# Optimization experiments

Hardware: AMD Instinct MI355X
Metric: run time of the kernel (lower is better)

The kernel has to match this reference:

```python
import jax, jax.numpy as jnp
import numpy as np
import math

S, B, D = 2048, 8, 256
HEADS = 8
DPROJ = 128
DFF = 1024
DH = DPROJ // HEADS  # 16


def _layernorm(x, g, b, eps=1e-5):
    mu = jnp.mean(x, axis=-1, keepdims=True)
    var = jnp.mean((x - mu) ** 2, axis=-1, keepdims=True)
    return (x - mu) * jax.lax.rsqrt(var + eps) * g + b


def setup_inputs() -> dict:
    key = jax.random.key(0)
    ks = jax.random.split(key, 16)
    s = 0.02
    return {
        "src": jax.random.normal(ks[0], (S, B, D), dtype=jnp.float32),
        "Wq": jax.random.normal(ks[1], (D, DPROJ), dtype=jnp.float32) * s,
        "bq": jnp.zeros((DPROJ,), dtype=jnp.float32),
        "Wk": jax.random.normal(ks[2], (D, DPROJ), dtype=jnp.float32) * s,
        "bk": jnp.zeros((DPROJ,), dtype=jnp.float32),
        "Wv": jax.random.normal(ks[3], (D, DPROJ), dtype=jnp.float32) * s,
        "bv": jnp.zeros((DPROJ,), dtype=jnp.float32),
        "Wo": jax.random.normal(ks[4], (DPROJ, D), dtype=jnp.float32) * s,
        "ln1_g": jnp.ones((D,), dtype=jnp.float32),
        "ln1_b": jnp.zeros((D,), dtype=jnp.float32),
        "W1": jax.random.normal(ks[5], (D, DFF), dtype=jnp.float32) * s,
        "b1": jnp.zeros((DFF,), dtype=jnp.float32),
        "W2": jax.random.normal(ks[6], (DFF, D), dtype=jnp.float32) * s,
        "b2": jnp.zeros((D,), dtype=jnp.float32),
        "ln2_g": jnp.ones((D,), dtype=jnp.float32),
        "ln2_b": jnp.zeros((D,), dtype=jnp.float32),
    }


def reference(src, Wq, bq, Wk, bk, Wv, bv, Wo, ln1_g, ln1_b, W1, b1, W2, b2, ln2_g, ln2_b):
    # src: (S, B, D)
    q = src @ Wq + bq  # (S, B, DPROJ)
    k = src @ Wk + bk
    v = src @ Wv + bv

    # _reshape_to_batches: (S, B, h*dh) -> (S, B*h, dh), then sdpa moves batch first
    def split_heads(x):
        return jnp.transpose(x.reshape(S, B * HEADS, DH), (1, 0, 2))  # (B*h, S, dh)

    qh, kh, vh = split_heads(q), split_heads(k), split_heads(v)
    scores = jnp.einsum('bid,bjd->bij', qh, kh) / math.sqrt(DH)  # (B*h, S, S)
    attn = jax.nn.softmax(scores, axis=-1)
    ctx = jnp.einsum('bij,bjd->bid', attn, vh)  # (B*h, S, dh)

    # _reshape_from_batches: (B*h, S, dh) -> (S, B, DPROJ)
    ctx = jnp.transpose(ctx, (1, 0, 2)).reshape(S, B, DPROJ)
    y = ctx @ Wo  # (S, B, D), no bias

    x = _layernorm(src + y, ln1_g, ln1_b)
    ffn = jax.nn.relu(x @ W1 + b1) @ W2 + b2
    return _layernorm(x + ffn, ln2_g, ln2_b)
```

## Files before the change

### kernel.cpp

```cpp
#include <hip/hip_runtime.h>
#include <math.h>

#define SLEN 2048
#define BATCH 8
#define DMODEL 256
#define HEADS 8
#define DPROJ 128
#define DFF 1024
#define DH 16
#define MROWS (SLEN*BATCH)

typedef unsigned short u16;
typedef unsigned int u32;
typedef __attribute__((ext_vector_type(8))) short short8;
typedef __attribute__((ext_vector_type(4))) short short4v;
typedef __attribute__((ext_vector_type(4))) float f32x4;
typedef __attribute__((ext_vector_type(4))) unsigned short u16x4;

__device__ __forceinline__ u16 f2bf(float x) {
    union { float f; u32 u; } v; v.f = x;
    u32 r = v.u + 0x7FFFu + ((v.u >> 16) & 1u);
    return (u16)(r >> 16);
}
__device__ __forceinline__ float bf2f(u16 h) {
    union { u32 u; float f; } v; v.u = ((u32)h) << 16;
    return v.f;
}
__device__ __forceinline__ float fexp2(float x) { return __builtin_amdgcn_exp2f(x); }
__device__ __forceinline__ short8 lds_short8_b64(const u16* p) {
    short4v lo = *(const short4v*)p;
    short4v hi = *(const short4v*)(p + 4);
    return __builtin_shufflevector(lo, hi, 0, 1, 2, 3, 4, 5, 6, 7);
}

__global__ void conv_src_kernel(const float* __restrict__ src, u16* __restrict__ dst) {
    int idx = (blockIdx.x * 256 + threadIdx.x) * 4;
    float4 v = *(const float4*)(src + idx);
    u16x4 o;
    o.x = f2bf(v.x); o.y = f2bf(v.y); o.z = f2bf(v.z); o.w = f2bf(v.w);
    *(u16x4*)(dst + idx) = o;
}

__global__ void conv_wts_kernel(const float* __restrict__ Wq, const float* __restrict__ Wk,
                                const float* __restrict__ Wv, const float* __restrict__ Wo,
                                const float* __restrict__ W1, const float* __restrict__ W2,
                                u16* __restrict__ WqT, u16* __restrict__ WkT,
                                u16* __restrict__ WvT, u16* __restrict__ WoT,
                                u16* __restrict__ W1T, u16* __restrict__ W2T) {
    int i = blockIdx.x * 256 + threadIdx.x;
    if (i < 32768) {
        int n = i >> 8, k = i & 255;
        WqT[i] = f2bf(Wq[k * 128 + n]);
    } else if (i < 65536) {
        int j = i - 32768; int n = j >> 8, k = j & 255;
        WkT[j] = f2bf(Wk[k * 128 + n]);
    } else if (i < 98304) {
        int j = i - 65536; int n = j >> 8, k = j & 255;
        WvT[j] = f2bf(Wv[k * 128 + n]);
    } else if (i < 131072) {
        int j = i - 98304; int n = j >> 7, k = j & 127;
        WoT[j] = f2bf(Wo[k * 256 + n]);
    } else if (i < 393216) {
        int j = i - 131072; int n = j >> 8, k = j & 255;
        W1T[j] = f2bf(W1[k * 1024 + n]);
    } else if (i < 655360) {
        int j = i - 393216; int n = j >> 10, k = j & 1023;
        W2T[j] = f2bf(W2[k * 256 + n]);
    }
}

template<int BN, bool RELU, bool HAS_BIAS, bool OUT_BF16>
__global__ void mfma_gemm(const u16* __restrict__ A, const u16* __restrict__ BT,
                          const float* __restrict__ bias, void* __restrict__ Cout,
                          int M, int N, int K) {
    constexpr int NJ = BN / 32;
    __shared__ __align__(16) u16 As[128 * 40];
    __shared__ __align__(16) u16 Bs[BN * 40];
    const int tid = threadIdx.x;
    const int row0 = blockIdx.x * 128;
    const int col0 = blockIdx.y * BN;
    const int w = tid >> 6, l = tid & 63;
    const int wr = (w & 1) * 64, wc = (w >> 1) * (BN / 2);
    const int lcol = l & 15, lrow = (l >> 4) * 4, kq = (l >> 4) * 8;
    const int sr = tid >> 2;
    const int sc = (tid & 3) * 8;

    f32x4 acc[4][NJ] = {};
    for (int k0 = 0; k0 < K; k0 += 32) {
        *(uint4*)(As + sr * 40 + sc) =
            *(const uint4*)(A + (size_t)(row0 + sr) * K + k0 + sc);
        *(uint4*)(As + (sr + 64) * 40 + sc) =
            *(const uint4*)(A + (size_t)(row0 + sr + 64) * K + k0 + sc);
        *(uint4*)(Bs + sr * 40 + sc) =
            *(const uint4*)(BT + (size_t)(col0 + sr) * K + k0 + sc);
        if (BN == 128)
            *(uint4*)(Bs + (sr + 64) * 40 + sc) =
                *(const uint4*)(BT + (size_t)(col0 + sr + 64) * K + k0 + sc);
        __syncthreads();
        short8 af[4], bf[NJ];
        #pragma unroll
        for (int i = 0; i < 4; ++i)
            af[i] = *(const short8*)(As + (wr + i * 16 + lcol) * 40 + kq);
        #pragma unroll
        for (int j = 0; j < NJ; ++j)
            bf[j] = *(const short8*)(Bs + (wc + j * 16 + lcol) * 40 + kq);
        #pragma unroll
        for (int i = 0; i < 4; ++i)
            #pragma unroll
            for (int j = 0; j < NJ; ++j)
                acc[i][j] = __builtin_amdgcn_mfma_f32_16x16x32_bf16(
                    af[i], bf[j], acc[i][j], 0, 0, 0);
        __syncthreads();
    }
    float bv[NJ];
    #pragma unroll
    for (int j = 0; j < NJ; ++j)
        bv[j] = HAS_BIAS ? bias[col0 + wc + j * 16 + lcol] : 0.f;
    #pragma unroll
    for (int i = 0; i < 4; ++i) {
        #pragma unroll
        for (int r = 0; r < 4; ++r) {
            size_t grow = row0 + wr + i * 16 + lrow + r;
            #pragma unroll
            for (int j = 0; j < NJ; ++j) {
                int gcol = col0 + wc + j * 16 + lcol;
                float c = acc[i][j][r] + bv[j];
                if (RELU) c = fmaxf(c, 0.f);
                if (OUT_BF16) ((u16*)Cout)[grow * N + gcol] = f2bf(c);
                else          ((float*)Cout)[grow * N + gcol] = c;
            }
        }
    }
}

__global__ void qkv_mfma(const u16* __restrict__ A,
                         const u16* __restrict__ WqT, const u16* __restrict__ WkT,
                         const u16* __restrict__ WvT,
                         const float* __restrict__ bq, const float* __restrict__ bk,
                         const float* __restrict__ bv,
                         u16* __restrict__ qhp, u16* __restrict__ khp,
                         u16* __restrict__ vhb) {
    const int which = blockIdx.z;
    const u16* BT   = which == 0 ? WqT : (which == 1 ? WkT : WvT);
    const float* bs = which == 0 ? bq : (which == 1 ? bk : bv);
    const float scale = which == 0 ? 0.25f * 1.44269504f : 1.0f;
    __shared__ __align__(16) u16 As[128 * 40];
    __shared__ __align__(16) u16 Bs[128 * 40];
    const int tid = threadIdx.x;
    const int row0 = blockIdx.x * 128;
    const int w = tid >> 6, l = tid & 63;
    const int wr = (w & 1) * 64, wc = (w >> 1) * 64;
    const int lcol = l & 15, lrow = (l >> 4) * 4, kq = (l >> 4) * 8;
    const int sr = tid >> 2;
    const int sc = (tid & 3) * 8;

    f32x4 acc[4][4] = {};
    for (int k0 = 0; k0 < DMODEL; k0 += 32) {
        *(uint4*)(As + sr * 40 + sc) =
            *(const uint4*)(A + (size_t)(row0 + sr) * DMODEL + k0 + sc);
        *(uint4*)(As + (sr + 64) * 40 + sc) =
            *(const uint4*)(A + (size_t)(row0 + sr + 64) * DMODEL + k0 + sc);
        *(uint4*)(Bs + sr * 40 + sc) =
            *(const uint4*)(BT + (size_t)sr * DMODEL + k0 + sc);
        *(uint4*)(Bs + (sr + 64) * 40 + sc) =
            *(const uint4*)(BT + (size_t)(sr + 64) * DMODEL + k0 + sc);
        __syncthreads();
        short8 af[4], bf[4];
        #pragma unroll
        for (int i = 0; i < 4; ++i)
            af[i] = *(const short8*)(As + (wr + i * 16 + lcol) * 40 + kq);
        #pragma unroll
        for (int j = 0; j < 4; ++j)
            bf[j] = *(const short8*)(Bs + (wc + j * 16 + lcol) * 40 + kq);
        #pragma unroll
        for (int i = 0; i < 4; ++i)
            #pragma unroll
            for (int j = 0; j < 4; ++j)
                acc[i][j] = __builtin_amdgcn_mfma_f32_16x16x32_bf16(
                    af[i], bf[j], acc[i][j], 0, 0, 0);
        __syncthreads();
    }
    #pragma unroll
    for (int i = 0; i < 4; ++i) {
        #pragma unroll
        for (int r = 0; r < 4; ++r) {
            int grow = row0 + wr + i * 16 + lrow + r;
            int b = grow & 7, s = grow >> 3;
            #pragma unroll
            for (int j = 0; j < 4; ++j) {
                int gcol = wc + j * 16 + lcol;
                int h = gcol >> 4, d = gcol & 15;
                float c = acc[i][j][r] + bs[gcol];
                if (which == 2) {
                    vhb[((size_t)(b * 8 + h) * SLEN + s) * 16 + d] = f2bf(c);
                } else {
                    u16* base = (which == 0 ? qhp : khp)
                              + ((size_t)(b * 8 + h) * SLEN + s) * 32;
                    base[d] = f2bf(c * scale);
                    base[d + 16] = 0;
                }
            }
        }
    }
}

__global__ __launch_bounds__(256, 4)
void attn_mfma(const u16* __restrict__ qg, const u16* __restrict__ kg,
               const u16* __restrict__ vg, u16* __restrict__ ctx) {
    __shared__ __align__(16) u16 Qs[128 * 40];
    __shared__ __align__(16) u16 Ksm[64 * 40];
    __shared__ __align__(16) u16 VTs[16 * 68];
    __shared__ __align__(16) u16 Ps[4 * 32 * 68];
    const int bh = blockIdx.y;
    const int q0 = blockIdx.x * 128;
    const int tid = threadIdx.x;
    const int w = tid >> 6, l = tid & 63;
    const int lcol = l & 15, lrow4 = (l >> 4) * 4, kq = (l >> 4) * 8;
    u16* Pw = Ps + w * (32 * 68);

    {
        const u16* qbase = qg + ((size_t)bh * SLEN + q0) * 32;
        #pragma unroll
        for (int it = 0; it < 2; ++it) {
            int idx = tid + it * 256;
            int row = idx >> 2, c = (idx & 3) * 8;
            *(uint4*)(Qs + row * 40 + c) = *(const uint4*)(qbase + row * 32 + c);
        }
    }

    f32x4 o_[2] = {};
    f32x4 ls[2] = {};
    const short one_bf = (short)0x3F80;
    short8 onesB = {one_bf, one_bf, one_bf, one_bf, one_bf, one_bf, one_bf, one_bf};

    const int srow = tid >> 2, sc8 = (tid & 3) * 8;
    const int vkey = tid & 63, vd4 = (tid >> 6) * 4;

    for (int k0 = 0; k0 < SLEN; k0 += 64) {
        __syncthreads();
        *(uint4*)(Ksm + srow * 40 + sc8) =
            *(const uint4*)(kg + ((size_t)bh * SLEN + k0 + srow) * 32 + sc8);
        {
            uint2 vv = *(const uint2*)(vg + ((size_t)bh * SLEN + k0 + vkey) * 16 + vd4);
            VTs[(vd4 + 0) * 68 + vkey] = (u16)(vv.x & 0xffff);
            VTs[(vd4 + 1) * 68 + vkey] = (u16)(vv.x >> 16);
            VTs[(vd4 + 2) * 68 + vkey] = (u16)(vv.y & 0xffff);
            VTs[(vd4 + 3) * 68 + vkey] = (u16)(vv.y >> 16);
        }
        __syncthreads();

        short8 aq[2];
        #pragma unroll
        for (int mi = 0; mi < 2; ++mi)
            aq[mi] = *(const short8*)(Qs + (w * 32 + mi * 16 + lcol) * 40 + kq);
        f32x4 s_[2][4];
        #pragma unroll
        for (int nj = 0; nj < 4; ++nj) {
            short8 bk_ = *(const short8*)(Ksm + (nj * 16 + lcol) * 40 + kq);
            #pragma unroll
            for (int mi = 0; mi < 2; ++mi) {
                f32x4 z = {0.f, 0.f, 0.f, 0.f};
                s_[mi][nj] = __builtin_amdgcn_mfma_f32_16x16x32_bf16(aq[mi], bk_, z, 0, 0, 0);
            }
        }
        #pragma unroll
        for (int mi = 0; mi < 2; ++mi)
            #pragma unroll
            for (int nj = 0; nj < 4; ++nj)
                #pragma unroll
                for (int r = 0; r < 4; ++r)
                    Pw[(mi * 16 + lrow4 + r) * 68 + nj * 16 + lcol] =
                        f2bf(fexp2(s_[mi][nj][r]));
        #pragma unroll
        for (int ks = 0; ks < 2; ++ks) {
            short8 bv_ = lds_short8_b64(VTs + lcol * 68 + ks * 32 + kq);
            #pragma unroll
            for (int mi = 0; mi < 2; ++mi) {
                short8 ap = lds_short8_b64(Pw + (mi * 16 + lcol) * 68 + ks * 32 + kq);
                o_[mi] = __builtin_amdgcn_mfma_f32_16x16x32_bf16(ap, bv_, o_[mi], 0, 0, 0);
                ls[mi] = __builtin_amdgcn_mfma_f32_16x16x32_bf16(ap, onesB, ls[mi], 0, 0, 0);
            }
        }
    }
    const int b = bh >> 3, h = bh & 7;
    #pragma unroll
    for (int mi = 0; mi < 2; ++mi)
        #pragma unroll
        for (int r = 0; r < 4; ++r) {
            int qrow = q0 + w * 32 + mi * 16 + lrow4 + r;
            ctx[((size_t)qrow * BATCH + b) * DPROJ + h * DH + lcol] =
                f2bf(o_[mi][r] / ls[mi][r]);
        }
}

__global__ void ln1_kernel(const float* __restrict__ src, const u16* __restrict__ y,
                           const float* __restrict__ g, const float* __restrict__ bb,
                           u16* __restrict__ xb) {
    const int w = threadIdx.x >> 6, l = threadIdx.x & 63;
    const int row = blockIdx.x * 4 + w;
    const int c = l * 4;
    size_t base = (size_t)row * DMODEL;
    float4 s4 = *(const float4*)(src + base + c);
    u16x4 y4 = *(const u16x4*)(y + base + c);
    float v[4] = { s4.x + bf2f(y4.x), s4.y + bf2f(y4.y),
                   s4.z + bf2f(y4.z), s4.w + bf2f(y4.w) };
    float sum = v[0] + v[1] + v[2] + v[3];
    float ss  = v[0]*v[0] + v[1]*v[1] + v[2]*v[2] + v[3]*v[3];
    #pragma unroll
    for (int off = 1; off < 64; off <<= 1) {
        sum += __shfl_xor(sum, off);
        ss  += __shfl_xor(ss, off);
    }
    float mu = sum * (1.0f / 256.0f);
    float var = ss * (1.0f / 256.0f) - mu * mu;
    float rs = rsqrtf(var + 1e-5f);
    float4 g4 = *(const float4*)(g + c);
    float4 b4 = *(const float4*)(bb + c);
    u16x4 o;
    o.x = f2bf((v[0] - mu) * rs * g4.x + b4.x);
    o.y = f2bf((v[1] - mu) * rs * g4.y + b4.y);
    o.z = f2bf((v[2] - mu) * rs * g4.z + b4.z);
    o.w = f2bf((v[3] - mu) * rs * g4.w + b4.w);
    *(u16x4*)(xb + base + c) = o;
}

__global__ void ln2_kernel(const u16* __restrict__ x, const u16* __restrict__ f,
                           const float* __restrict__ g, const float* __restrict__ bb,
                           float* __restrict__ out) {
    const int w = threadIdx.x >> 6, l = threadIdx.x & 63;
    const int row = blockIdx.x * 4 + w;
    const int c = l * 4;
    size_t base = (size_t)row * DMODEL;
    u16x4 x4 = *(const u16x4*)(x + base + c);
    u16x4 f4 = *(const u16x4*)(f + base + c);
    float v[4] = { bf2f(x4.x) + bf2f(f4.x), bf2f(x4.y) + bf2f(f4.y),
                   bf2f(x4.z) + bf2f(f4.z), bf2f(x4.w) + bf2f(f4.w) };
    float sum = v[0] + v[1] + v[2] + v[3];
    float ss  = v[0]*v[0] + v[1]*v[1] + v[2]*v[2] + v[3]*v[3];
    #pragma unroll
    for (int off = 1; off < 64; off <<= 1) {
        sum += __shfl_xor(sum, off);
        ss  += __shfl_xor(ss, off);
    }
    float mu = sum * (1.0f / 256.0f);
    float var = ss * (1.0f / 256.0f) - mu * mu;
    float rs = rsqrtf(var + 1e-5f);
    float4 g4 = *(const float4*)(g + c);
    float4 b4 = *(const float4*)(bb + c);
    float4 o;
    o.x = (v[0] - mu) * rs * g4.x + b4.x;
    o.y = (v[1] - mu) * rs * g4.y + b4.y;
    o.z = (v[2] - mu) * rs * g4.z + b4.z;
    o.w = (v[3] - mu) * rs * g4.w + b4.w;
    *(float4*)(out + base + c) = o;
}

extern "C" void kernel_launch(void* const* d_in, const int* in_sizes, int n_in,
                              void* d_out, int out_size, void* d_ws, size_t ws_size,
                              hipStream_t stream) {
    const float* src = (const float*)d_in[0];
    const float* Wq  = (const float*)d_in[1];
    const float* bq  = (const float*)d_in[2];
    const float* Wk  = (const float*)d_in[3];
    const float* bk  = (const float*)d_in[4];
    const float* Wv  = (const float*)d_in[5];
    const float* bv  = (const float*)d_in[6];
    const float* Wo  = (const float*)d_in[7];
    const float* g1  = (const float*)d_in[8];
    const float* be1 = (const float*)d_in[9];
    const float* W1  = (const float*)d_in[10];
    const float* b1  = (const float*)d_in[11];
    const float* W2  = (const float*)d_in[12];
    const float* b2  = (const float*)d_in[13];
    const float* g2  = (const float*)d_in[14];
    const float* be2 = (const float*)d_in[15];
    char* ws = (char*)d_ws;
    float* out = (float*)d_out;

    u16* qhp  = (u16*)(ws + 0);
    u16* khp  = (u16*)(ws + 8388608);
    u16* vhb  = (u16*)(ws + 16777216);
    u16* ctxb = (u16*)(ws + 20971520);
    u16* yb   = (u16*)(ws + 25165824);
    u16* hb   = (u16*)(ws + 0);
    u16* xb   = (u16*)(ws + 33554432);
    u16* fb   = (u16*)(ws + 41943040);
    u16* srcb = (u16*)(ws + 50331648);
    u16* WqT  = (u16*)(ws + 58720256);
    u16* WkT  = (u16*)(ws + 58785792);
    u16* WvT  = (u16*)(ws + 58851328);
    u16* WoT  = (u16*)(ws + 58916864);
    u16* W1T  = (u16*)(ws + 58982400);
    u16* W2T  = (u16*)(ws + 59506688);

    conv_src_kernel<<<4096, 256, 0, stream>>>(src, srcb);
    conv_wts_kernel<<<2560, 256, 0, stream>>>(Wq, Wk, Wv, Wo, W1, W2,
                                              WqT, WkT, WvT, WoT, W1T, W2T);
    qkv_mfma<<<dim3(128, 1, 3), 256, 0, stream>>>(srcb, WqT, WkT, WvT,
                                                  bq, bk, bv, qhp, khp, vhb);
    attn_mfma<<<dim3(16, 64), 256, 0, stream>>>(qhp, khp, vhb, ctxb);
    mfma_gemm<64, false, false, true><<<dim3(128, 4), 256, 0, stream>>>(
        ctxb, WoT, nullptr, yb, MROWS, DMODEL, DPROJ);
    ln1_kernel<<<MROWS / 4, 256, 0, stream>>>(src, yb, g1, be1, xb);
    mfma_gemm<128, true, true, true><<<dim3(128, 8), 256, 0, stream>>>(
        xb, W1T, b1, hb, MROWS, DFF, DMODEL);
    mfma_gemm<64, false, true, true><<<dim3(128, 4), 256, 0, stream>>>(
        hb, W2T, b2, fb, MROWS, DMODEL, DFF);
    ln2_kernel<<<MROWS / 4, 256, 0, stream>>>(xb, fb, g2, be2, out);
}
```

Measured before the change: 246.9 us.

## Load attention K/V fragments directly from global and pre-transpose V

Adds a separate kernel that transposes V into a per-head [d][key] layout. The attention kernel now loads Q, K and V MFMA fragments straight from global memory into registers, dropping the shared-memory K/V staging and both block-wide barriers per key tile. It computes S^T (K as the A operand) so the exp'd probabilities can be packed two bf16 per u32 with a perm instruction and written to LDS as wider stores. The cost is an extra kernel launch plus the V transpose traffic, and uncoalesced, repeated global (L2) fragment loads by every wave.

```diff
diff --git a/kernel.cpp b/kernel.cpp
--- a/kernel.cpp
+++ b/kernel.cpp
@@ -13,7 +13,6 @@
 typedef unsigned short u16;
 typedef unsigned int u32;
 typedef __attribute__((ext_vector_type(8))) short short8;
-typedef __attribute__((ext_vector_type(4))) short short4v;
 typedef __attribute__((ext_vector_type(4))) float f32x4;
 typedef __attribute__((ext_vector_type(4))) unsigned short u16x4;
 
@@ -22,15 +21,10 @@
     u32 r = v.u + 0x7FFFu + ((v.u >> 16) & 1u);
     return (u16)(r >> 16);
 }
-__device__ __forceinline__ float bf2f(u16 h) {
-    union { u32 u; float f; } v; v.u = ((u32)h) << 16;
-    return v.f;
-}
 __device__ __forceinline__ float fexp2(float x) { return __builtin_amdgcn_exp2f(x); }
-__device__ __forceinline__ short8 lds_short8_b64(const u16* p) {
-    short4v lo = *(const short4v*)p;
-    short4v hi = *(const short4v*)(p + 4);
-    return __builtin_shufflevector(lo, hi, 0, 1, 2, 3, 4, 5, 6, 7);
+__device__ __forceinline__ u32 pack_bf(float lo, float hi) {
+    union { float f; u32 u; } a, b; a.f = lo; b.f = hi;
+    return __builtin_amdgcn_perm(b.u, a.u, 0x07060302u);
 }
 
 __global__ void conv_src_kernel(const float* __restrict__ src, u16* __restrict__ dst) {
@@ -204,95 +198,109 @@
     }
 }
 
+__global__ void transpose_v(const u16* __restrict__ vhb, u16* __restrict__ vT) {
+    __shared__ u16 T[128 * 24];
+    const int bh = blockIdx.y;
+    const int c0 = blockIdx.x * 128;
+    const int t = threadIdx.x;
+    {
+        int key = t >> 1, half = t & 1;
+        *(uint4*)(T + key * 24 + half * 8) =
+            *(const uint4*)(vhb + ((size_t)bh * SLEN + c0 + key) * 16 + half * 8);
+    }
+    __syncthreads();
+    int d = t >> 4, k8 = (t & 15) * 8;
+    u16x4 o0, o1;
+    o0.x = T[(k8 + 0) * 24 + d]; o0.y = T[(k8 + 1) * 24 + d];
+    o0.z = T[(k8 + 2) * 24 + d]; o0.w = T[(k8 + 3) * 24 + d];
+    o1.x = T[(k8 + 4) * 24 + d]; o1.y = T[(k8 + 5) * 24 + d];
+    o1.z = T[(k8 + 6) * 24 + d]; o1.w = T[(k8 + 7) * 24 + d];
+    u16* dst = vT + ((size_t)bh * 16 + d) * SLEN + c0 + k8;
+    *(u16x4*)dst = o0;
+    *(u16x4*)(dst + 4) = o1;
+}
+
 __global__ __launch_bounds__(256, 4)
 void attn_mfma(const u16* __restrict__ qg, const u16* __restrict__ kg,
-               const u16* __restrict__ vg, u16* __restrict__ ctx) {
-    __shared__ __align__(16) u16 Qs[128 * 40];
-    __shared__ __align__(16) u16 Ksm[64 * 40];
-    __shared__ __align__(16) u16 VTs[16 * 68];
-    __shared__ __align__(16) u16 Ps[4 * 32 * 68];
+               const u16* __restrict__ vT, u16* __restrict__ ctx) {
+    __shared__ __align__(16) u16 Ps[4 * 32 * 70];
     const int bh = blockIdx.y;
     const int q0 = blockIdx.x * 128;
     const int tid = threadIdx.x;
     const int w = tid >> 6, l = tid & 63;
-    const int lcol = l & 15, lrow4 = (l >> 4) * 4, kq = (l >> 4) * 8;
-    u16* Pw = Ps + w * (32 * 68);
-
+    const int qc = l & 15, g = l >> 4;
+    u16* Pw = Ps + w * (32 * 70);
+
+    short8 qf[2];
     {
-        const u16* qbase = qg + ((size_t)bh * SLEN + q0) * 32;
-        #pragma unroll
-        for (int it = 0; it < 2; ++it) {
-            int idx = tid + it * 256;
-            int row = idx >> 2, c = (idx & 3) * 8;
-            *(uint4*)(Qs + row * 40 + c) = *(const uint4*)(qbase + row * 32 + c);
-        }
-    }
+        const u16* qbase = qg + ((size_t)bh * SLEN + q0 + w * 32) * 32;
+        qf[0] = *(const short8*)(qbase + qc * 32 + 8 * g);
+        qf[1] = *(const short8*)(qbase + (16 + qc) * 32 + 8 * g);
+    }
+    const u16* kbase = kg + (size_t)bh * SLEN * 32;
+    const u16* vbase = vT + ((size_t)bh * 16 + qc) * SLEN;
 
     f32x4 o_[2] = {};
     f32x4 ls[2] = {};
     const short one_bf = (short)0x3F80;
     short8 onesB = {one_bf, one_bf, one_bf, one_bf, one_bf, one_bf, one_bf, one_bf};
 
-    const int srow = tid >> 2, sc8 = (tid & 3) * 8;
-    const int vkey = tid & 63, vd4 = (tid >> 6) * 4;
-
     for (int k0 = 0; k0 < SLEN; k0 += 64) {
-        __syncthreads();
-        *(uint4*)(Ksm + srow * 40 + sc8) =
-            *(const uint4*)(kg + ((size_t)bh * SLEN + k0 + srow) * 32 + sc8);
-        {
-            uint2 vv = *(const uint2*)(vg + ((size_t)bh * SLEN + k0 + vkey) * 16 + vd4);
-            VTs[(vd4 + 0) * 68 + vkey] = (u16)(vv.x & 0xffff);
-            VTs[(vd4 + 1) * 68 + vkey] = (u16)(vv.x >> 16);
-            VTs[(vd4 + 2) * 68 + vkey] = (u16)(vv.y & 0xffff);
-            VTs[(vd4 + 3) * 68 + vkey] = (u16)(vv.y >> 16);
-        }
-        __syncthreads();
-
-        short8 aq[2];
-        #pragma unroll
-        for (int mi = 0; mi < 2; ++mi)
-            aq[mi] = *(const short8*)(Qs + (w * 32 + mi * 16 + lcol) * 40 + kq);
-        f32x4 s_[2][4];
-        #pragma unroll
-        for (int nj = 0; nj < 4; ++nj) {
-            short8 bk_ = *(const short8*)(Ksm + (nj * 16 + lcol) * 40 + kq);
+        short8 kf[4], vf[2];
+        #pragma unroll
+        for (int kj = 0; kj < 4; ++kj)
+            kf[kj] = *(const short8*)(kbase + (size_t)(k0 + kj * 16 + qc) * 32 + 8 * g);
+        #pragma unroll
+        for (int ks = 0; ks < 2; ++ks)
+            vf[ks] = *(const short8*)(vbase + k0 + ks * 32 + 8 * g);
+
+        f32x4 s_[4][2];
+        #pragma unroll
+        for (int kj = 0; kj < 4; ++kj)
             #pragma unroll
             for (int mi = 0; mi < 2; ++mi) {
                 f32x4 z = {0.f, 0.f, 0.f, 0.f};
-                s_[mi][nj] = __builtin_amdgcn_mfma_f32_16x16x32_bf16(aq[mi], bk_, z, 0, 0, 0);
+                s_[kj][mi] = __builtin_amdgcn_mfma_f32_16x16x32_bf16(
+                    kf[kj], qf[mi], z, 0, 0, 0);
+            }
+        #pragma unroll
+        for (int mi = 0; mi < 2; ++mi)
+            #pragma unroll
+            for (int kj = 0; kj < 4; ++kj) {
+                f32x4 sv = s_[kj][mi];
+                u32 d0 = pack_bf(fexp2(sv[0]), fexp2(sv[1]));
+                u32 d1 = pack_bf(fexp2(sv[2]), fexp2(sv[3]));
+                u32* pp = (u32*)(Pw + (mi * 16 + qc) * 70 + kj * 16 + 4 * g);
+                pp[0] = d0;
+                pp[1] = d1;
+            }
+        #pragma unroll
+        for (int ks = 0; ks < 2; ++ks) {
+            #pragma unroll
+            for (int mi = 0; mi < 2; ++mi) {
+                const u32* rp = (const u32*)(Pw + (mi * 16 + qc) * 70 + ks * 32 + 8 * g);
+                union { u32 d[4]; short8 v; } ap;
+                ap.d[0] = rp[0]; ap.d[1] = rp[1]; ap.d[2] = rp[2]; ap.d[3] = rp[3];
+                o_[mi] = __builtin_amdgcn_mfma_f32_16x16x32_bf16(ap.v, vf[ks], o_[mi], 0, 0, 0);
+                ls[mi] = __builtin_amdgcn_mfma_f32_16x16x32_bf16(ap.v, onesB, ls[mi], 0, 0, 0);
             }
         }
-        #pragma unroll
-        for (int mi = 0; mi < 2; ++mi)
-            #pragma unroll
-            for (int nj = 0; nj < 4; ++nj)
-                #pragma unroll
-                for (int r = 0; r < 4; ++r)
-                    Pw[(mi * 16 + lrow4 + r) * 68 + nj * 16 + lcol] =
-                        f2bf(fexp2(s_[mi][nj][r]));
-        #pragma unroll
-        for (int ks = 0; ks < 2; ++ks) {
-            short8 bv_ = lds_short8_b64(VTs + lcol * 68 + ks * 32 + kq);
-            #pragma unroll
-            for (int mi = 0; mi < 2; ++mi) {
-                short8 ap = lds_short8_b64(Pw + (mi * 16 + lcol) * 68 + ks * 32 + kq);
-                o_[mi] = __builtin_amdgcn_mfma_f32_16x16x32_bf16(ap, bv_, o_[mi], 0, 0, 0);
-                ls[mi] = __builtin_amdgcn_mfma_f32_16x16x32_bf16(ap, onesB, ls[mi], 0, 0, 0);
-            }
-        }
     }
     const int b = bh >> 3, h = bh & 7;
     #pragma unroll
     for (int mi = 0; mi < 2; ++mi)
         #pragma unroll
         for (int r = 0; r < 4; ++r) {
-            int qrow = q0 + w * 32 + mi * 16 + lrow4 + r;
-            ctx[((size_t)qrow * BATCH + b) * DPROJ + h * DH + lcol] =
+            int qrow = q0 + w * 32 + mi * 16 + 4 * g + r;
+            ctx[((size_t)qrow * BATCH + b) * DPROJ + h * DH + qc] =
                 f2bf(o_[mi][r] / ls[mi][r]);
         }
 }
 
+__device__ __forceinline__ float bf2f(u16 h) {
+    union { u32 u; float f; } v; v.u = ((u32)h) << 16;
+    return v.f;
+}
 __global__ void ln1_kernel(const float* __restrict__ src, const u16* __restrict__ y,
                            const float* __restrict__ g, const float* __restrict__ bb,
                            u16* __restrict__ xb) {
@@ -380,25 +388,27 @@
     u16* qhp  = (u16*)(ws + 0);
     u16* khp  = (u16*)(ws + 8388608);
     u16* vhb  = (u16*)(ws + 16777216);
-    u16* ctxb = (u16*)(ws + 20971520);
-    u16* yb   = (u16*)(ws + 25165824);
+    u16* vT   = (u16*)(ws + 20971520);
+    u16* ctxb = (u16*)(ws + 25165824);
+    u16* yb   = (u16*)(ws + 29360128);
     u16* hb   = (u16*)(ws + 0);
-    u16* xb   = (u16*)(ws + 33554432);
-    u16* fb   = (u16*)(ws + 41943040);
-    u16* srcb = (u16*)(ws + 50331648);
-    u16* WqT  = (u16*)(ws + 58720256);
-    u16* WkT  = (u16*)(ws + 58785792);
-    u16* WvT  = (u16*)(ws + 58851328);
-    u16* WoT  = (u16*)(ws + 58916864);
-    u16* W1T  = (u16*)(ws + 58982400);
-    u16* W2T  = (u16*)(ws + 59506688);
+    u16* xb   = (u16*)(ws + 37748736);
+    u16* fb   = (u16*)(ws + 46137344);
+    u16* srcb = (u16*)(ws + 54525952);
+    u16* WqT  = (u16*)(ws + 62914560);
+    u16* WkT  = (u16*)(ws + 62980096);
+    u16* WvT  = (u16*)(ws + 63045632);
+    u16* WoT  = (u16*)(ws + 63111168);
+    u16* W1T  = (u16*)(ws + 63176704);
+    u16* W2T  = (u16*)(ws + 63700992);
 
     conv_src_kernel<<<4096, 256, 0, stream>>>(src, srcb);
     conv_wts_kernel<<<2560, 256, 0, stream>>>(Wq, Wk, Wv, Wo, W1, W2,
                                               WqT, WkT, WvT, WoT, W1T, W2T);
     qkv_mfma<<<dim3(128, 1, 3), 256, 0, stream>>>(srcb, WqT, WkT, WvT,
                                                   bq, bk, bv, qhp, khp, vhb);
-    attn_mfma<<<dim3(16, 64), 256, 0, stream>>>(qhp, khp, vhb, ctxb);
+    transpose_v<<<dim3(16, 64), 256, 0, stream>>>(vhb, vT);
+    attn_mfma<<<dim3(16, 64), 256, 0, stream>>>(qhp, khp, vT, ctxb);
     mfma_gemm<64, false, false, true><<<dim3(128, 4), 256, 0, stream>>>(
         ctxb, WoT, nullptr, yb, MROWS, DMODEL, DPROJ);
     ln1_kernel<<<MROWS / 4, 256, 0, stream>>>(src, yb, g1, be1, xb);
```

After: 235.9 us. 1.05x faster.
